# Performance work log

Hardware: AMD Instinct MI355X
Metric: run time of the kernel (lower is better)

## Reference

```python
import jax, jax.numpy as jnp
import numpy as np

N_EMBED = 1024
NUM_HEADS = 16
HEAD_SIZE = 64  # NUM_HEADS * HEAD_SIZE == N_EMBED
BLOCK_SIZE = 2048


def setup_inputs() -> dict:
    key = jax.random.key(0)
    ks = jax.random.split(key, 9)
    s = 1.0 / np.sqrt(N_EMBED)
    batch_x = jax.random.normal(ks[0], (4, BLOCK_SIZE, N_EMBED), dtype=jnp.float32)
    # stacked per-head linear params: weight [H, E, d], bias [H, d]
    Wq = jax.random.uniform(ks[1], (NUM_HEADS, N_EMBED, HEAD_SIZE), jnp.float32, -s, s)
    Wk = jax.random.uniform(ks[2], (NUM_HEADS, N_EMBED, HEAD_SIZE), jnp.float32, -s, s)
    Wv = jax.random.uniform(ks[3], (NUM_HEADS, N_EMBED, HEAD_SIZE), jnp.float32, -s, s)
    bq = jax.random.uniform(ks[4], (NUM_HEADS, HEAD_SIZE), jnp.float32, -s, s)
    bk = jax.random.uniform(ks[5], (NUM_HEADS, HEAD_SIZE), jnp.float32, -s, s)
    bv = jax.random.uniform(ks[6], (NUM_HEADS, HEAD_SIZE), jnp.float32, -s, s)
    Wp = jax.random.uniform(ks[7], (N_EMBED, N_EMBED), jnp.float32, -s, s)
    bp = jax.random.uniform(ks[8], (N_EMBED,), jnp.float32, -s, s)
    return {"batch_x": batch_x, "Wq": Wq, "Wk": Wk, "Wv": Wv,
            "bq": bq, "bk": bk, "bv": bv, "Wp": Wp, "bp": bp}


def reference(batch_x, Wq, Wk, Wv, bq, bk, bv, Wp, bp):
    B, T, E = batch_x.shape
    # per-head projections: [B, H, T, d]
    q = jnp.einsum('bte,hed->bhtd', batch_x, Wq) + bq[None, :, None, :]
    k = jnp.einsum('bte,hed->bhtd', batch_x, Wk) + bk[None, :, None, :]
    v = jnp.einsum('bte,hed->bhtd', batch_x, Wv) + bv[None, :, None, :]
    scale = 1.0 / jnp.sqrt(jnp.asarray(HEAD_SIZE, batch_x.dtype))
    wei = jnp.einsum('bhtd,bhsd->bhts', q, k) * scale  # [B,H,T,T]
    causal = jnp.tril(jnp.ones((T, T), dtype=bool))
    wei = jnp.where(causal, wei, jnp.asarray(-jnp.inf, wei.dtype))
    wei = jax.nn.softmax(wei, axis=-1)
    out = jnp.einsum('bhts,bhsd->bhtd', wei, v)  # [B,H,T,d]
    # concat heads (head order matches torch.cat over ModuleList)
    out = out.transpose(0, 2, 1, 3).reshape(B, T, NUM_HEADS * HEAD_SIZE)
    return out @ Wp + bp
```

## Files before the change

kernel.cpp:

```cpp
#include <hip/hip_runtime.h>
#include <math.h>

#define B_ 4
#define T_ 2048
#define E_ 1024
#define H_ 16
#define D_ 64

typedef __bf16 bf16_t;
typedef bf16_t bf16x8 __attribute__((ext_vector_type(8)));
typedef float  f32x4  __attribute__((ext_vector_type(4)));
typedef float  f32x16 __attribute__((ext_vector_type(16)));
typedef unsigned short u16x4 __attribute__((ext_vector_type(4)));

static __device__ __forceinline__ unsigned short f2bf(float f) {
    bf16_t h = (bf16_t)f;
    return __builtin_bit_cast(unsigned short, h);
}

#define GLD(gp, lp) __builtin_amdgcn_global_load_lds( \
    (const __attribute__((address_space(1))) unsigned int*)(gp), \
    (__attribute__((address_space(3))) unsigned int*)(lp), 16, 0, 0)

#define BAR() __builtin_amdgcn_s_barrier()
#define WAIT_LGKM0() asm volatile("s_waitcnt lgkmcnt(0)" ::: "memory")

__global__ void cast_x_kernel(const float* __restrict__ in, unsigned short* __restrict__ out, int n4) {
    int i = blockIdx.x * blockDim.x + threadIdx.x;
    if (i >= n4) return;
    float4 v = ((const float4*)in)[i];
    ushort4 o;
    o.x = f2bf(v.x); o.y = f2bf(v.y); o.z = f2bf(v.z); o.w = f2bf(v.w);
    ((ushort4*)out)[i] = o;
}

__global__ void tcast_all(const float* __restrict__ Wq, const float* __restrict__ Wk,
                          const float* __restrict__ Wv, const float* __restrict__ Wp,
                          unsigned short* __restrict__ wf, unsigned short* __restrict__ wpt) {
    __shared__ unsigned short Ts[64 * 66];
    const int grp = blockIdx.y >> 4, yy = blockIdx.y & 15;
    const float* in; unsigned short* out; int yA, S;
    if (grp == 3) { in = Wp; out = wpt; yA = 64;    S = 1024; }
    else {
        in = (grp == 0) ? Wq : (grp == 1) ? Wk : Wv;
        out = wf + (size_t)grp * 1024 * 1024; yA = 65536; S = 64;
    }
    const int tid = threadIdx.x;
    const int r = tid >> 2, c4 = tid & 3;
    const float* ip = in + (size_t)yA * yy + (size_t)(blockIdx.x * 64 + r) * S + c4 * 16;
    #pragma unroll
    for (int j = 0; j < 4; ++j) {
        float4 v = *(const float4*)&ip[j * 4];
        Ts[(c4 * 16 + j * 4 + 0) * 66 + r] = f2bf(v.x);
        Ts[(c4 * 16 + j * 4 + 1) * 66 + r] = f2bf(v.y);
        Ts[(c4 * 16 + j * 4 + 2) * 66 + r] = f2bf(v.z);
        Ts[(c4 * 16 + j * 4 + 3) * 66 + r] = f2bf(v.w);
    }
    __syncthreads();
    unsigned short* op = out + (size_t)(yy * 64 + r) * 1024 + blockIdx.x * 64 + c4 * 16;
    #pragma unroll
    for (int j = 0; j < 4; ++j) {
        u16x4 pk;
        #pragma unroll
        for (int m = 0; m < 4; ++m) pk[m] = Ts[r * 66 + c4 * 16 + j * 4 + m];
        *(u16x4*)&op[j * 4] = pk;
    }
}

__global__ __launch_bounds__(512, 2) void qkv_gemm(
    const unsigned short* __restrict__ xb,
    const unsigned short* __restrict__ wf,
    const float* __restrict__ bq, const float* __restrict__ bk, const float* __restrict__ bv,
    unsigned short* __restrict__ qo, unsigned short* __restrict__ ko,
    unsigned short* __restrict__ vt)
{
    __shared__ __align__(16) unsigned short sm[65536];

    const int tid = threadIdx.x;
    const int w = tid >> 6, lane = tid & 63;
    const int wr = w >> 2, wc = w & 3;
    const int l15 = lane & 15, quad = lane >> 4, lsw = l15 & 7;
    const int m0 = blockIdx.x * 256;
    const int n0 = blockIdx.y * 256;

    f32x4 acc[8][4];
    #pragma unroll
    for (int i = 0; i < 8; ++i)
        #pragma unroll
        for (int j = 0; j < 4; ++j) acc[i][j] = (f32x4){0.f, 0.f, 0.f, 0.f};

    const int swzE = (((lane & 7) ^ (lane >> 3)) * 8);
    const unsigned short* Agb = xb + (size_t)(m0 + (lane >> 3)) * 1024 + swzE;
    const unsigned short* Bgb = wf + (size_t)(n0 + (lane >> 3)) * 1024 + swzE;

    auto stage = [&](int t, int q) {
        unsigned short* Ad = sm + q * 32768 + w * 512;
        unsigned short* Bd = Ad + 16384;
        const unsigned short* Ag = Agb + t * 64;
        const unsigned short* Bg = Bgb + t * 64;
        #pragma unroll
        for (int j = 0; j < 4; ++j) {
            GLD(Ag + (size_t)(j * 64 + w * 8) * 1024, Ad + j * 4096);
            GLD(Bg + (size_t)(j * 64 + w * 8) * 1024, Bd + j * 4096);
        }
    };
    auto rdA = [&](const unsigned short* Ad, int fm, int ks) {
        return *(const bf16x8*)&Ad[(wr * 128 + fm * 16 + l15) * 64 + (((ks * 4 + quad) ^ lsw) * 8)];
    };
    auto rdB = [&](const unsigned short* Bd, int fn, int ks) {
        return *(const bf16x8*)&Bd[(wc * 64 + fn * 16 + l15) * 64 + (((ks * 4 + quad) ^ lsw) * 8)];
    };

    stage(0, 0);
    stage(1, 1);
    asm volatile("s_waitcnt vmcnt(8)" ::: "memory");
    BAR();

    for (int T = 0; T < 16; ++T) {
        const unsigned short* Ad = sm + (T & 1) * 32768;
        const unsigned short* Bd = Ad + 16384;
        bf16x8 fA[4][2], fB[4][2];

        #pragma unroll
        for (int i = 0; i < 4; ++i) { fA[i][0] = rdA(Ad, i, 0); fA[i][1] = rdA(Ad, i, 1); }
        #pragma unroll
        for (int j = 0; j < 2; ++j) { fB[j][0] = rdB(Bd, j, 0); fB[j][1] = rdB(Bd, j, 1); }
        BAR(); WAIT_LGKM0();
        __builtin_amdgcn_s_setprio(1);
        #pragma unroll
        for (int i = 0; i < 4; ++i)
            #pragma unroll
            for (int j = 0; j < 2; ++j)
                #pragma unroll
                for (int ks = 0; ks < 2; ++ks)
                    acc[i][j] = __builtin_amdgcn_mfma_f32_16x16x32_bf16(fA[i][ks], fB[j][ks], acc[i][j], 0, 0, 0);
        __builtin_amdgcn_s_setprio(0);
        BAR();

        #pragma unroll
        for (int j = 0; j < 2; ++j) { fB[2 + j][0] = rdB(Bd, 2 + j, 0); fB[2 + j][1] = rdB(Bd, 2 + j, 1); }
        BAR(); WAIT_LGKM0();
        __builtin_amdgcn_s_setprio(1);
        #pragma unroll
        for (int i = 0; i < 4; ++i)
            #pragma unroll
            for (int j = 0; j < 2; ++j)
                #pragma unroll
                for (int ks = 0; ks < 2; ++ks)
                    acc[i][2 + j] = __builtin_amdgcn_mfma_f32_16x16x32_bf16(fA[i][ks], fB[2 + j][ks], acc[i][2 + j], 0, 0, 0);
        __builtin_amdgcn_s_setprio(0);
        BAR();

        #pragma unroll
        for (int i = 0; i < 4; ++i) { fA[i][0] = rdA(Ad, 4 + i, 0); fA[i][1] = rdA(Ad, 4 + i, 1); }
        BAR(); WAIT_LGKM0();
        __builtin_amdgcn_s_setprio(1);
        #pragma unroll
        for (int i = 0; i < 4; ++i)
            #pragma unroll
            for (int j = 0; j < 2; ++j)
                #pragma unroll
                for (int ks = 0; ks < 2; ++ks)
                    acc[4 + i][2 + j] = __builtin_amdgcn_mfma_f32_16x16x32_bf16(fA[i][ks], fB[2 + j][ks], acc[4 + i][2 + j], 0, 0, 0);
        __builtin_amdgcn_s_setprio(0);
        BAR();

        if (T < 14) {
            stage(T + 2, T & 1);
            asm volatile("s_waitcnt vmcnt(8)" ::: "memory");
        } else {
            asm volatile("s_waitcnt vmcnt(0)" ::: "memory");
        }
        BAR();
        __builtin_amdgcn_s_setprio(1);
        #pragma unroll
        for (int i = 0; i < 4; ++i)
            #pragma unroll
            for (int j = 0; j < 2; ++j)
                #pragma unroll
                for (int ks = 0; ks < 2; ++ks)
                    acc[4 + i][j] = __builtin_amdgcn_mfma_f32_16x16x32_bf16(fA[i][ks], fB[j][ks], acc[4 + i][j], 0, 0, 0);
        __builtin_amdgcn_s_setprio(0);
        BAR();
    }

    const int which = n0 >> 10;
    const int nb = n0 & 1023;
    if (which < 2) {
        const float* bias = which ? bk : bq;
        unsigned short* outp = which ? ko : qo;
        const float sc = which ? 1.f : 0.125f;
        #pragma unroll
        for (int fm = 0; fm < 8; ++fm)
            #pragma unroll
            for (int fn = 0; fn < 4; ++fn) {
                int colg = nb + wc * 64 + fn * 16 + l15;
                int h = colg >> 6, d = colg & 63;
                float bi = bias[colg];
                #pragma unroll
                for (int r = 0; r < 4; ++r) {
                    int row = m0 + wr * 128 + fm * 16 + quad * 4 + r;
                    int b = row >> 11, t = row & 2047;
                    outp[(((size_t)b * 16 + h) * 2048 + t) * 64 + d] = f2bf((acc[fm][fn][r] + bi) * sc);
                }
            }
    } else {
        const int b = m0 >> 11;
        for (int mh = 0; mh < 2; ++mh)
            for (int nh = 0; nh < 2; ++nh) {
                __syncthreads();
                if (wr == mh && (wc >> 1) == nh) {
                    const int cc = wc & 1;
                    #pragma unroll
                    for (int fm = 0; fm < 8; ++fm)
                        #pragma unroll
                        for (int fn = 0; fn < 4; ++fn) {
                            int colL = cc * 64 + fn * 16 + l15;
                            int colg = nb + nh * 128 + colL;
                            float bi = bv[colg];
                            u16x4 pk;
                            #pragma unroll
                            for (int r = 0; r < 4; ++r) pk[r] = f2bf(acc[fm][fn][r] + bi);
                            *(u16x4*)&sm[colL * 136 + fm * 16 + quad * 4] = pk;
                        }
                }
                __syncthreads();
                const int nl = tid >> 2, tq = tid & 3;
                const int colg = nb + nh * 128 + nl;
                const int h = colg >> 6, d = colg & 63;
                const int t0 = (m0 & 2047) + mh * 128;
                unsigned short* dst = vt + (((size_t)b * 16 + h) * 64 + d) * 2048 + t0 + tq * 32;
                #pragma unroll
                for (int j = 0; j < 4; ++j)
                    *(float4*)&dst[j * 8] = *(const float4*)&sm[nl * 136 + tq * 32 + j * 8];
            }
    }
}

__global__ __launch_bounds__(256, 3) void attn_kernel(
    const unsigned short* __restrict__ q, const unsigned short* __restrict__ k,
    const unsigned short* __restrict__ vt, unsigned short* __restrict__ att2)
{
    __shared__ __align__(16) unsigned short Ks[64 * 64];
    __shared__ __align__(16) unsigned short Vs[64 * 64];
    __shared__ __align__(16) unsigned short Ps[4][32 * 64];

    const int tid = threadIdx.x;
    const int w = tid >> 6, lane = tid & 63;
    const int l31 = lane & 31, h = lane >> 5;
    const int bh = blockIdx.x;
    const int sw_q = l31 & 7;

    unsigned short* Pw = Ps[w];
    const unsigned short* kb = k  + (size_t)bh * 2048 * 64;
    const unsigned short* vb = vt + (size_t)bh * 64 * 2048;
    const int sr = tid >> 2;
    const int sc0 = tid & 3;
    const int ssw = sr & 7;

    for (int leg = 0; leg < 2; ++leg) {
        const int qtile = leg ? (15 - (int)blockIdx.y) : (int)blockIdx.y;
        const int qb0 = qtile * 128;
        const int qg = qb0 + w * 32 + l31;
        const int qmin = qb0 + w * 32, qmax = qmin + 31;
        const int trips = 2 * qtile + 2;

        bf16x8 fQ[4];
        {
            const unsigned short* qp = q + ((size_t)bh * 2048 + qg) * 64 + h * 8;
            #pragma unroll
            for (int ks = 0; ks < 4; ++ks) fQ[ks] = *(const bf16x8*)&qp[ks * 16];
        }

        f32x16 O[2];
        #pragma unroll
        for (int nt = 0; nt < 2; ++nt)
            #pragma unroll
            for (int i = 0; i < 16; ++i) O[nt][i] = 0.f;
        float lsum = 0.f;

        for (int jt = 0; jt < trips; ++jt) {
            __syncthreads();
            {
                const unsigned short* kg = kb + (size_t)(jt * 64) * 64;
                const unsigned short* vg = vb + jt * 64;
                #pragma unroll
                for (int it = 0; it < 2; ++it) {
                    int ci = sc0 + 4 * it;
                    int sw = ((ci ^ ssw)) * 8;
                    *(float4*)&Ks[sr * 64 + sw] = *(const float4*)&kg[(size_t)sr * 64 + ci * 8];
                    *(float4*)&Vs[sr * 64 + sw] = *(const float4*)&vg[(size_t)sr * 2048 + ci * 8];
                }
            }
            __syncthreads();

            const int key0 = jt * 64;
            if (key0 <= qmax) {
                f32x16 S[2];
                #pragma unroll
                for (int kt = 0; kt < 2; ++kt)
                    #pragma unroll
                    for (int i = 0; i < 16; ++i) S[kt][i] = 0.f;
                __builtin_amdgcn_s_setprio(1);
                #pragma unroll
                for (int kt = 0; kt < 2; ++kt) {
                    const int row = kt * 32 + l31, rs = row & 7;
                    #pragma unroll
                    for (int ks = 0; ks < 4; ++ks) {
                        bf16x8 aK = *(const bf16x8*)&Ks[row * 64 + ((2 * ks + h) ^ rs) * 8];
                        S[kt] = __builtin_amdgcn_mfma_f32_32x32x16_bf16(aK, fQ[ks], S[kt], 0, 0, 0);
                    }
                }
                __builtin_amdgcn_s_setprio(0);

                const bool need_mask = (key0 + 63) > qmin;
                #pragma unroll
                for (int kt = 0; kt < 2; ++kt) {
                    #pragma unroll
                    for (int g = 0; g < 4; ++g) {
                        u16x4 pk;
                        #pragma unroll
                        for (int r = 0; r < 4; ++r) {
                            float p = __expf(S[kt][4 * g + r]);
                            if (need_mask) {
                                int key = key0 + kt * 32 + 8 * g + 4 * h + r;
                                if (key > qg) p = 0.f;
                            }
                            lsum += p;
                            pk[r] = f2bf(p);
                        }
                        *(u16x4*)&Pw[l31 * 64 + ((4 * kt + g) ^ sw_q) * 8 + 4 * h] = pk;
                    }
                }
                __builtin_amdgcn_s_setprio(1);
                #pragma unroll
                for (int ks2 = 0; ks2 < 4; ++ks2) {
                    bf16x8 aP = *(const bf16x8*)&Pw[l31 * 64 + ((2 * ks2 + h) ^ sw_q) * 8];
                    #pragma unroll
                    for (int nt = 0; nt < 2; ++nt) {
                        const int drow = nt * 32 + l31;
                        bf16x8 bV = *(const bf16x8*)&Vs[drow * 64 + ((2 * ks2 + h) ^ (drow & 7)) * 8];
                        O[nt] = __builtin_amdgcn_mfma_f32_32x32x16_bf16(aP, bV, O[nt], 0, 0, 0);
                    }
                }
                __builtin_amdgcn_s_setprio(0);
            }
        }

        lsum += __shfl_xor(lsum, 32);
        const float inv = 1.f / lsum;

        unsigned short* ob = att2 + ((size_t)bh * 2048 + qb0 + w * 32) * 64;
        #pragma unroll
        for (int g = 0; g < 4; ++g)
            #pragma unroll
            for (int r = 0; r < 4; ++r) {
                const int qy = 8 * g + 4 * h + r;
                const float iv = __shfl(inv, qy);
                #pragma unroll
                for (int nt = 0; nt < 2; ++nt)
                    ob[(size_t)qy * 64 + nt * 32 + l31] = f2bf(O[nt][4 * g + r] * iv);
            }
    }
}

__global__ __launch_bounds__(256) void proj_gemm(
    const unsigned short* __restrict__ A,
    const unsigned short* __restrict__ wpt,
    const float* __restrict__ bp,
    float* __restrict__ out)
{
    __shared__ __align__(16) unsigned short sm[16384];
    unsigned short* As = sm;
    unsigned short* Bs = sm + 8192;

    const int tid = threadIdx.x;
    const int w = tid >> 6, lane = tid & 63, l15 = lane & 15, quad = lane >> 4;
    const int m0 = blockIdx.x * 128;
    const int n0 = blockIdx.y * 128;

    f32x4 acc[2][8];
    #pragma unroll
    for (int s = 0; s < 2; ++s)
        #pragma unroll
        for (int n = 0; n < 8; ++n) acc[s][n] = (f32x4){0.f, 0.f, 0.f, 0.f};

    const unsigned short* Ag = A + (size_t)(m0 >> 11) * 16 * 131072
                                 + (size_t)((m0 & 2047) + 32 * w + (lane >> 3)) * 64 + (lane & 7) * 8;
    const unsigned short* Bg = wpt + (size_t)(n0 + 32 * w + (lane >> 3)) * 1024 + (lane & 7) * 8;
    unsigned short* Al = As + (32 * w) * 64;
    unsigned short* Bl = Bs + (32 * w) * 64;

    for (int k0 = 0; k0 < 1024; k0 += 64) {
        __syncthreads();
        const size_t aoff = (size_t)(k0 >> 6) * 131072;
        #pragma unroll
        for (int j = 0; j < 4; ++j) {
            GLD(Ag + aoff + (size_t)(8 * j) * 64, Al + (8 * j) * 64);
            GLD(Bg + (size_t)(8 * j) * 1024 + k0, Bl + (8 * j) * 64);
        }
        __syncthreads();
        #pragma unroll
        for (int ks = 0; ks < 2; ++ks) {
            bf16x8 a0 = *(const bf16x8*)&As[(32 * w + l15) * 64 + ks * 32 + quad * 8];
            bf16x8 a1 = *(const bf16x8*)&As[(32 * w + 16 + l15) * 64 + ks * 32 + quad * 8];
            #pragma unroll
            for (int n = 0; n < 8; ++n) {
                bf16x8 b = *(const bf16x8*)&Bs[(16 * n + l15) * 64 + ks * 32 + quad * 8];
                acc[0][n] = __builtin_amdgcn_mfma_f32_16x16x32_bf16(a0, b, acc[0][n], 0, 0, 0);
                acc[1][n] = __builtin_amdgcn_mfma_f32_16x16x32_bf16(a1, b, acc[1][n], 0, 0, 0);
            }
        }
    }

    #pragma unroll
    for (int s = 0; s < 2; ++s)
        #pragma unroll
        for (int n = 0; n < 8; ++n) {
            float bi = bp[n0 + 16 * n + l15];
            #pragma unroll
            for (int r = 0; r < 4; ++r) {
                int row = m0 + 32 * w + 16 * s + quad * 4 + r;
                out[(size_t)row * 1024 + n0 + 16 * n + l15] = acc[s][n][r] + bi;
            }
        }
}

extern "C" void kernel_launch(void* const* d_in, const int* in_sizes, int n_in,
                              void* d_out, int out_size, void* d_ws, size_t ws_size,
                              hipStream_t stream) {
    const float* x  = (const float*)d_in[0];
    const float* Wq = (const float*)d_in[1];
    const float* Wk = (const float*)d_in[2];
    const float* Wv = (const float*)d_in[3];
    const float* bq = (const float*)d_in[4];
    const float* bk = (const float*)d_in[5];
    const float* bv = (const float*)d_in[6];
    const float* Wp = (const float*)d_in[7];
    const float* bp = (const float*)d_in[8];
    float* out = (float*)d_out;

    const size_t nx = (size_t)B_ * T_ * E_;
    unsigned short* base = (unsigned short*)d_ws;
    unsigned short* xb  = base;
    unsigned short* qb  = xb + nx;
    unsigned short* kb  = qb + nx;
    unsigned short* vtb = kb + nx;
    unsigned short* atb = vtb + nx;
    unsigned short* wf  = atb + nx;
    unsigned short* wpt = wf + 3072 * 1024;

    cast_x_kernel<<<(int)(nx / 4 + 255) / 256, 256, 0, stream>>>(x, xb, (int)(nx / 4));
    tcast_all<<<dim3(16, 64), 256, 0, stream>>>(Wq, Wk, Wv, Wp, wf, wpt);
    qkv_gemm<<<dim3(32, 12), 512, 0, stream>>>(xb, wf, bq, bk, bv, qb, kb, vtb);
    attn_kernel<<<dim3(64, 8), 256, 0, stream>>>(qb, kb, vtb, atb);
    proj_gemm<<<dim3(64, 8), 256, 0, stream>>>(atb, wpt, bp, out);
}
```

Measured before the change: 282.7 us.

## Interleave global-to-LDS staging in quarter chunks across MFMA phases of QKV GEMM

Restructures the QKV projection GEMM main loop so each K-tile's global_load_lds is split into four quarter-stages (A-low, A-high, B-low, B-high), issued one per MFMA phase instead of all at once. A quarter of the buffer is refilled as soon as it has been read into registers, keeping memory requests in flight continuously. The loop is unrolled by two tiles with an explicit vmcnt(4) wait. This adds more intricate buffer-reuse ordering and barrier reliance, which risks races if a quarter is overwritten before all waves have read it.

Result: faster. 273.0 us (-3.4%).

```diff
diff --git a/kernel.cpp b/kernel.cpp
--- a/kernel.cpp
+++ b/kernel.cpp
@@ -90,99 +90,117 @@
         for (int j = 0; j < 4; ++j) acc[i][j] = (f32x4){0.f, 0.f, 0.f, 0.f};
 
     const int swzE = (((lane & 7) ^ (lane >> 3)) * 8);
-    const unsigned short* Agb = xb + (size_t)(m0 + (lane >> 3)) * 1024 + swzE;
-    const unsigned short* Bgb = wf + (size_t)(n0 + (lane >> 3)) * 1024 + swzE;
-
-    auto stage = [&](int t, int q) {
-        unsigned short* Ad = sm + q * 32768 + w * 512;
-        unsigned short* Bd = Ad + 16384;
-        const unsigned short* Ag = Agb + t * 64;
-        const unsigned short* Bg = Bgb + t * 64;
-        #pragma unroll
-        for (int j = 0; j < 4; ++j) {
-            GLD(Ag + (size_t)(j * 64 + w * 8) * 1024, Ad + j * 4096);
-            GLD(Bg + (size_t)(j * 64 + w * 8) * 1024, Bd + j * 4096);
-        }
+    const unsigned short* Agb = xb + (size_t)(m0 + w * 16 + (lane >> 3)) * 1024 + swzE;
+    const unsigned short* Bgb = wf + (size_t)(n0 + w * 16 + (lane >> 3)) * 1024 + swzE;
+
+    auto stage_half = [&](int t, int which) {
+        unsigned short* dst = sm + (t & 1) * 32768 + which * 8192 + w * 1024;
+        const unsigned short* src = ((which < 2) ? Agb : Bgb)
+                                  + (size_t)((which & 1) * 128) * 1024 + t * 64;
+        GLD(src, dst);
+        GLD(src + (size_t)8 * 1024, dst + 512);
     };
-    auto rdA = [&](const unsigned short* Ad, int fm, int ks) {
-        return *(const bf16x8*)&Ad[(wr * 128 + fm * 16 + l15) * 64 + (((ks * 4 + quad) ^ lsw) * 8)];
+    auto rdA = [&](int t, int fm, int ks) {
+        const int row = wr * 128 + fm * 16 + l15;
+        return *(const bf16x8*)&sm[(t & 1) * 32768 + (row >> 7) * 8192
+                                   + (row & 127) * 64 + (((ks * 4 + quad) ^ lsw) * 8)];
     };
-    auto rdB = [&](const unsigned short* Bd, int fn, int ks) {
-        return *(const bf16x8*)&Bd[(wc * 64 + fn * 16 + l15) * 64 + (((ks * 4 + quad) ^ lsw) * 8)];
+    auto rdB = [&](int t, int fn, int ks) {
+        const int row = wc * 64 + fn * 16 + l15;
+        return *(const bf16x8*)&sm[(t & 1) * 32768 + 16384 + (row >> 7) * 8192
+                                   + (row & 127) * 64 + (((ks * 4 + quad) ^ lsw) * 8)];
     };
 
-    stage(0, 0);
-    stage(1, 1);
-    asm volatile("s_waitcnt vmcnt(8)" ::: "memory");
+    stage_half(0, 0); stage_half(0, 1); stage_half(0, 2); stage_half(0, 3);
+    stage_half(1, 2); stage_half(1, 3);
+    asm volatile("s_waitcnt vmcnt(4)" ::: "memory");
     BAR();
 
-    for (int T = 0; T < 16; ++T) {
-        const unsigned short* Ad = sm + (T & 1) * 32768;
-        const unsigned short* Bd = Ad + 16384;
+    #define MFMA_Q(mb, nb) \
+        __builtin_amdgcn_s_setprio(1); \
+        _Pragma("unroll") \
+        for (int i_ = 0; i_ < 4; ++i_) \
+            _Pragma("unroll") \
+            for (int j_ = 0; j_ < 2; ++j_) \
+                _Pragma("unroll") \
+                for (int ks_ = 0; ks_ < 2; ++ks_) \
+                    acc[(mb) + i_][(nb) + j_] = __builtin_amdgcn_mfma_f32_16x16x32_bf16( \
+                        fA[i_][ks_], fB[(nb) + j_][ks_], acc[(mb) + i_][(nb) + j_], 0, 0, 0); \
+        __builtin_amdgcn_s_setprio(0);
+
+    #pragma unroll 1
+    for (int it = 0; it < 8; ++it) {
+        const int t0 = 2 * it, t1 = 2 * it + 1;
+        const bool more = it < 7;
         bf16x8 fA[4][2], fB[4][2];
 
         #pragma unroll
-        for (int i = 0; i < 4; ++i) { fA[i][0] = rdA(Ad, i, 0); fA[i][1] = rdA(Ad, i, 1); }
-        #pragma unroll
-        for (int j = 0; j < 2; ++j) { fB[j][0] = rdB(Bd, j, 0); fB[j][1] = rdB(Bd, j, 1); }
-        BAR(); WAIT_LGKM0();
-        __builtin_amdgcn_s_setprio(1);
-        #pragma unroll
-        for (int i = 0; i < 4; ++i)
-            #pragma unroll
-            for (int j = 0; j < 2; ++j)
-                #pragma unroll
-                for (int ks = 0; ks < 2; ++ks)
-                    acc[i][j] = __builtin_amdgcn_mfma_f32_16x16x32_bf16(fA[i][ks], fB[j][ks], acc[i][j], 0, 0, 0);
-        __builtin_amdgcn_s_setprio(0);
-        BAR();
-
-        #pragma unroll
-        for (int j = 0; j < 2; ++j) { fB[2 + j][0] = rdB(Bd, 2 + j, 0); fB[2 + j][1] = rdB(Bd, 2 + j, 1); }
-        BAR(); WAIT_LGKM0();
-        __builtin_amdgcn_s_setprio(1);
-        #pragma unroll
-        for (int i = 0; i < 4; ++i)
-            #pragma unroll
-            for (int j = 0; j < 2; ++j)
-                #pragma unroll
-                for (int ks = 0; ks < 2; ++ks)
-                    acc[i][2 + j] = __builtin_amdgcn_mfma_f32_16x16x32_bf16(fA[i][ks], fB[2 + j][ks], acc[i][2 + j], 0, 0, 0);
-        __builtin_amdgcn_s_setprio(0);
-        BAR();
-
-        #pragma unroll
-        for (int i = 0; i < 4; ++i) { fA[i][0] = rdA(Ad, 4 + i, 0); fA[i][1] = rdA(Ad, 4 + i, 1); }
-        BAR(); WAIT_LGKM0();
-        __builtin_amdgcn_s_setprio(1);
-        #pragma unroll
-        for (int i = 0; i < 4; ++i)
-            #pragma unroll
-            for (int j = 0; j < 2; ++j)
-                #pragma unroll
-                for (int ks = 0; ks < 2; ++ks)
-                    acc[4 + i][2 + j] = __builtin_amdgcn_mfma_f32_16x16x32_bf16(fA[i][ks], fB[2 + j][ks], acc[4 + i][2 + j], 0, 0, 0);
-        __builtin_amdgcn_s_setprio(0);
-        BAR();
-
-        if (T < 14) {
-            stage(T + 2, T & 1);
-            asm volatile("s_waitcnt vmcnt(8)" ::: "memory");
+        for (int m = 0; m < 4; ++m) { fA[m][0] = rdA(t0, m, 0); fA[m][1] = rdA(t0, m, 1); }
+        #pragma unroll
+        for (int n = 0; n < 2; ++n) { fB[n][0] = rdB(t0, n, 0); fB[n][1] = rdB(t0, n, 1); }
+        stage_half(t1, 0);
+        BAR(); WAIT_LGKM0();
+        MFMA_Q(0, 0);
+        BAR();
+
+        #pragma unroll
+        for (int n = 0; n < 2; ++n) { fB[2 + n][0] = rdB(t0, 2 + n, 0); fB[2 + n][1] = rdB(t0, 2 + n, 1); }
+        stage_half(t1, 1);
+        BAR(); WAIT_LGKM0();
+        MFMA_Q(0, 2);
+        BAR();
+
+        #pragma unroll
+        for (int m = 0; m < 4; ++m) { fA[m][0] = rdA(t0, 4 + m, 0); fA[m][1] = rdA(t0, 4 + m, 1); }
+        if (more) stage_half(t0 + 2, 2);
+        BAR(); WAIT_LGKM0();
+        MFMA_Q(4, 2);
+        BAR();
+
+        if (more) {
+            stage_half(t0 + 2, 3);
+            asm volatile("s_waitcnt vmcnt(4)" ::: "memory");
         } else {
             asm volatile("s_waitcnt vmcnt(0)" ::: "memory");
         }
         BAR();
-        __builtin_amdgcn_s_setprio(1);
-        #pragma unroll
-        for (int i = 0; i < 4; ++i)
-            #pragma unroll
-            for (int j = 0; j < 2; ++j)
-                #pragma unroll
-                for (int ks = 0; ks < 2; ++ks)
-                    acc[4 + i][j] = __builtin_amdgcn_mfma_f32_16x16x32_bf16(fA[i][ks], fB[j][ks], acc[4 + i][j], 0, 0, 0);
-        __builtin_amdgcn_s_setprio(0);
-        BAR();
-    }
+        MFMA_Q(4, 0);
+        BAR();
+
+        #pragma unroll
+        for (int m = 0; m < 4; ++m) { fA[m][0] = rdA(t1, m, 0); fA[m][1] = rdA(t1, m, 1); }
+        #pragma unroll
+        for (int n = 0; n < 2; ++n) { fB[n][0] = rdB(t1, n, 0); fB[n][1] = rdB(t1, n, 1); }
+        if (more) stage_half(t0 + 2, 0);
+        BAR(); WAIT_LGKM0();
+        MFMA_Q(0, 0);
+        BAR();
+
+        #pragma unroll
+        for (int n = 0; n < 2; ++n) { fB[2 + n][0] = rdB(t1, 2 + n, 0); fB[2 + n][1] = rdB(t1, 2 + n, 1); }
+        if (more) stage_half(t0 + 2, 1);
+        BAR(); WAIT_LGKM0();
+        MFMA_Q(0, 2);
+        BAR();
+
+        #pragma unroll
+        for (int m = 0; m < 4; ++m) { fA[m][0] = rdA(t1, 4 + m, 0); fA[m][1] = rdA(t1, 4 + m, 1); }
+        if (more) stage_half(t1 + 2, 2);
+        BAR(); WAIT_LGKM0();
+        MFMA_Q(4, 2);
+        BAR();
+
+        if (more) {
+            stage_half(t1 + 2, 3);
+            asm volatile("s_waitcnt vmcnt(4)" ::: "memory");
+        } else {
+            asm volatile("s_waitcnt vmcnt(0)" ::: "memory");
+        }
+        BAR();
+        MFMA_Q(4, 0);
+        BAR();
+    }
+    #undef MFMA_Q
 
     const int which = n0 >> 10;
     const int nb = n0 & 1023;
```
